# Kernel optimization log

Hardware: AMD Instinct MI355X
Metric: run time of the kernel (lower is better)

The kernel has to match this reference:

```python
import jax, jax.numpy as jnp
import numpy as np

N_NODES = 50000
N_EDGES = 600000
D = 128


def setup_inputs() -> dict:
    key = jax.random.key(0)
    k = jax.random.split(key, 6)
    x = jax.random.normal(k[0], (N_NODES, D), dtype=jnp.float32)
    edge_src = jax.random.randint(k[1], (N_EDGES,), 0, N_NODES, dtype=jnp.int64 if jax.config.jax_enable_x64 else jnp.int32)
    edge_dst = jax.random.randint(k[2], (N_EDGES,), 0, N_NODES, dtype=jnp.int64 if jax.config.jax_enable_x64 else jnp.int32)
    # message MLP: [h_src ; h_dst] (2D) -> D, update MLP: [h ; agg] (2D) -> D
    scale = 1.0 / np.sqrt(2 * D)
    W1 = jax.random.normal(k[3], (2 * D, D), dtype=jnp.float32) * scale
    b1 = jnp.zeros((D,), dtype=jnp.float32)
    W2 = jax.random.normal(k[4], (2 * D, D), dtype=jnp.float32) * scale
    b2 = jnp.zeros((D,), dtype=jnp.float32)
    return {"x": x, "edge_src": edge_src, "edge_dst": edge_dst,
            "W1": W1, "b1": b1, "W2": W2, "b2": b2}


def reference(x, edge_src, edge_dst, W1, b1, W2, b2):
    # gather endpoint features per edge: [E, 2D]
    pair = jnp.concatenate([x[edge_src], x[edge_dst]], axis=-1)
    # per-edge message MLP: [E, D]
    msg = jax.nn.relu(pair @ W1 + b1)
    # scatter-aggregate (sum) messages into destination nodes: [N, D]
    agg = jax.ops.segment_sum(msg, edge_dst, num_segments=N_NODES)
    # node update MLP with residual: [N, D]
    upd = jax.nn.relu(jnp.concatenate([x, agg], axis=-1) @ W2 + b2)
    return x + upd
```

## Files before the change

### kernel.cpp

```cpp
#include <hip/hip_runtime.h>
#include <stdint.h>


typedef __attribute__((ext_vector_type(8))) short short8;
typedef __attribute__((ext_vector_type(4))) float floatx4;

#define D 128

static __device__ __forceinline__ unsigned short f2bf(float f) {
    union { float f; unsigned int u; } v; v.f = f;
    unsigned int r = (v.u + 0x7fffu + ((v.u >> 16) & 1u)) >> 16;
    return (unsigned short)r;
}
static __device__ __forceinline__ float bflo(unsigned int u) {
    union { unsigned int u; float f; } v; v.u = u << 16; return v.f;
}
static __device__ __forceinline__ float bfhi(unsigned int u) {
    union { unsigned int u; float f; } v; v.u = u & 0xffff0000u; return v.f;
}

__global__ void k_convert_w(const float* __restrict__ W1, const float* __restrict__ W2,
                            unsigned short* __restrict__ w1f, unsigned short* __restrict__ w2f,
                            int* __restrict__ cursor, int N) {
    int gid = blockIdx.x * blockDim.x + threadIdx.x;
    if (gid < N) cursor[gid] = 0;
    if (gid < 32768) {
        int tid = gid;
        int j = tid & 7, lane = (tid >> 3) & 63, ct = (tid >> 9) & 15, kk = tid >> 13;
        int k = kk * 32 + (lane >> 4) * 8 + j;
        int c = ((ct >> 2) << 6) + ((lane & 15) << 2) + (ct & 3);
        float v = (c < 128) ? W1[k * 128 + c] : W1[(128 + k) * 128 + (c - 128)];
        w1f[tid] = f2bf(v);
    } else {
        int tid = gid - 32768;
        int j = tid & 7, lane = (tid >> 3) & 63, ct = (tid >> 9) & 7, kk = tid >> 12;
        int k = kk * 32 + (lane >> 4) * 8 + j;
        int c = ((ct >> 1) << 5) + ((lane & 15) << 1) + (ct & 1);
        w2f[tid] = f2bf(W2[k * 128 + c]);
    }
}

__global__ __launch_bounds__(256) void k_gemm1(
    const float* __restrict__ x,
    const unsigned short* __restrict__ w1f,
    const float* __restrict__ b1,
    unsigned short* __restrict__ xb,
    unsigned short* __restrict__ Ys,
    unsigned short* __restrict__ Yd,
    int N, int nTiles)
{
    const int tid = threadIdx.x, w = tid >> 6, lane = tid & 63;
    const int quad = lane >> 4, col = lane & 15;

    short8 wf[4][4];
#pragma unroll
    for (int kk = 0; kk < 4; kk++)
#pragma unroll
        for (int j = 0; j < 4; j++)
            wf[kk][j] = ((const short8*)w1f)[(kk * 16 + w * 4 + j) * 64 + lane];
    float4 bias = make_float4(0.f, 0.f, 0.f, 0.f);
    if (w >= 2) bias = *(const float4*)(b1 + (w - 2) * 64 + col * 4);
    unsigned short* Yhalf = (w < 2) ? Ys : Yd;
    const int cb = (w & 1) * 64;

    for (int t = blockIdx.x; t < nTiles; t += gridDim.x) {
        const int n0 = t * 16;
        const int nr = n0 + col;
        const float* xrow = x + (long)nr * D;
        floatx4 acc[4];
#pragma unroll
        for (int j = 0; j < 4; j++)
#pragma unroll
            for (int q = 0; q < 4; q++) acc[j][q] = 0.f;
#pragma unroll
        for (int kk = 0; kk < 4; kk++) {
            float4 f0 = *(const float4*)(xrow + kk * 32 + quad * 8);
            float4 f1 = *(const float4*)(xrow + kk * 32 + quad * 8 + 4);
            union { short8 s; unsigned int u[4]; } au;
            asm("v_cvt_pk_bf16_f32 %0, %1, %2" : "=v"(au.u[0]) : "v"(f0.x), "v"(f0.y));
            asm("v_cvt_pk_bf16_f32 %0, %1, %2" : "=v"(au.u[1]) : "v"(f0.z), "v"(f0.w));
            asm("v_cvt_pk_bf16_f32 %0, %1, %2" : "=v"(au.u[2]) : "v"(f1.x), "v"(f1.y));
            asm("v_cvt_pk_bf16_f32 %0, %1, %2" : "=v"(au.u[3]) : "v"(f1.z), "v"(f1.w));
            if (w == 0)
                *(short8*)(xb + (long)nr * D + kk * 32 + quad * 8) = au.s;
#pragma unroll
            for (int j = 0; j < 4; j++)
                acc[j] = __builtin_amdgcn_mfma_f32_16x16x32_bf16(au.s, wf[kk][j], acc[j], 0, 0, 0);
        }
#pragma unroll
        for (int r = 0; r < 4; r++) {
            int n = n0 + quad * 4 + r;
            ushort4 o;
            o.x = f2bf(acc[0][r] + bias.x);
            o.y = f2bf(acc[1][r] + bias.y);
            o.z = f2bf(acc[2][r] + bias.z);
            o.w = f2bf(acc[3][r] + bias.w);
            *(ushort4*)(Yhalf + (long)n * D + cb + col * 4) = o;
        }
    }
}

__global__ void k_hist(const int* __restrict__ dst, int* __restrict__ cnt, int E) {
    int i = blockIdx.x * blockDim.x + threadIdx.x;
    if (i < E) atomicAdd(&cnt[dst[i]], 1);
}

__global__ void k_scanA(const int* __restrict__ cnt, int* __restrict__ rowptr,
                        int* __restrict__ bsum, int N) {
    __shared__ int ws[16];
    int tid = threadIdx.x, i = blockIdx.x * 1024 + tid;
    int lane = tid & 63, wv = tid >> 6;
    int c = (i < N) ? cnt[i] : 0;
    int incl = c;
#pragma unroll
    for (int off = 1; off < 64; off <<= 1) {
        int t = __shfl_up(incl, off, 64);
        if (lane >= off) incl += t;
    }
    if (lane == 63) ws[wv] = incl;
    __syncthreads();
    if (wv == 0) {
        int v = (lane < 16) ? ws[lane] : 0;
        int s = v;
#pragma unroll
        for (int off = 1; off < 16; off <<= 1) {
            int t = __shfl_up(s, off, 64);
            if (lane >= off) s += t;
        }
        if (lane < 16) ws[lane] = s - v;
    }
    __syncthreads();
    if (i < N) rowptr[i] = incl - c + ws[wv];
    if (tid == 1023) bsum[blockIdx.x] = ws[15] + incl;
}

__global__ void k_scanC(int* __restrict__ rowptr, int* __restrict__ cursor,
                        const int* __restrict__ bsum, int N, int E, int nb) {
    __shared__ int off_s;
    int tid = threadIdx.x;
    int chunk = blockIdx.x >> 2;
    if (tid < 64) {
        int v = (tid < chunk && tid < nb) ? bsum[tid] : 0;
#pragma unroll
        for (int off = 32; off; off >>= 1) v += __shfl_down(v, off, 64);
        if (tid == 0) off_s = v;
    }
    __syncthreads();
    int i = blockIdx.x * 256 + tid;
    if (i < N) {
        int r = rowptr[i] + off_s;
        rowptr[i] = r;
        cursor[i] = r;
    }
    if (i == 0) rowptr[N] = E;
}

__global__ void k_scatter(const int* __restrict__ src, const int* __restrict__ dst,
                          int* __restrict__ cursor, int* __restrict__ ssrc, int E) {
    int i = blockIdx.x * blockDim.x + threadIdx.x;
    if (i < E) {
        int p = atomicAdd(&cursor[dst[i]], 1);
        ssrc[p] = src[i];
    }
}

__global__ __launch_bounds__(256) void k_agg(
    const unsigned short* __restrict__ Ys,
    const unsigned short* __restrict__ Yd,
    const int* __restrict__ rowptr,
    const int* __restrict__ ssrc,
    unsigned short* __restrict__ aggb, int N)
{
    int wv = blockIdx.x * 4 + (threadIdx.x >> 6);
    if (wv >= N) return;
    int lane = threadIdx.x & 63;
    int rp0 = rowptr[wv], rp1 = rowptr[wv + 1];
    unsigned int ydu = *(const unsigned int*)(Yd + (long)wv * D + lane * 2);
    float yd0 = bflo(ydu), yd1 = bfhi(ydu);
    float a0 = 0.f, a1 = 0.f;
    const unsigned short* ysl = Ys + lane * 2;
    int e = rp0;
    for (; e + 8 <= rp1; e += 8) {
        int s[8]; unsigned int u[8];
#pragma unroll
        for (int q = 0; q < 8; q++) s[q] = ssrc[e + q];
#pragma unroll
        for (int q = 0; q < 8; q++) u[q] = *(const unsigned int*)(ysl + (long)s[q] * D);
#pragma unroll
        for (int q = 0; q < 8; q++) {
            a0 += fmaxf(bflo(u[q]) + yd0, 0.f);
            a1 += fmaxf(bfhi(u[q]) + yd1, 0.f);
        }
    }
    for (; e + 4 <= rp1; e += 4) {
        int s[4]; unsigned int u[4];
#pragma unroll
        for (int q = 0; q < 4; q++) s[q] = ssrc[e + q];
#pragma unroll
        for (int q = 0; q < 4; q++) u[q] = *(const unsigned int*)(ysl + (long)s[q] * D);
#pragma unroll
        for (int q = 0; q < 4; q++) {
            a0 += fmaxf(bflo(u[q]) + yd0, 0.f);
            a1 += fmaxf(bfhi(u[q]) + yd1, 0.f);
        }
    }
    for (; e < rp1; e++) {
        unsigned int u0 = *(const unsigned int*)(ysl + (long)ssrc[e] * D);
        a0 += fmaxf(bflo(u0) + yd0, 0.f);
        a1 += fmaxf(bfhi(u0) + yd1, 0.f);
    }
    unsigned int o = (unsigned int)f2bf(a0) | ((unsigned int)f2bf(a1) << 16);
    *(unsigned int*)(aggb + (long)wv * D + lane * 2) = o;
}

__global__ __launch_bounds__(256) void k_gemm2(
    const unsigned short* __restrict__ xb,
    const unsigned short* __restrict__ aggb,
    const unsigned short* __restrict__ w2f,
    const float* __restrict__ b2,
    const float* __restrict__ x,
    float* __restrict__ out,
    int N, int nTiles)
{
    const int tid = threadIdx.x, w = tid >> 6, lane = tid & 63;
    const int quad = lane >> 4, col = lane & 15;

    short8 wf[8][2];
#pragma unroll
    for (int kk = 0; kk < 8; kk++)
#pragma unroll
        for (int c = 0; c < 2; c++)
            wf[kk][c] = ((const short8*)w2f)[(kk * 8 + w * 2 + c) * 64 + lane];
    float2 bias = *(const float2*)(b2 + w * 32 + col * 2);

    for (int t = blockIdx.x; t < nTiles; t += gridDim.x) {
        const int n0 = t * 16;
        const int nr = n0 + col;
        floatx4 acc[2];
#pragma unroll
        for (int c = 0; c < 2; c++)
#pragma unroll
            for (int q = 0; q < 4; q++) acc[c][q] = 0.f;
#pragma unroll
        for (int kk = 0; kk < 8; kk++) {
            const unsigned short* base = (kk < 4) ? xb : aggb;
            short8 a = *(const short8*)(base + (long)nr * D + (kk & 3) * 32 + quad * 8);
            acc[0] = __builtin_amdgcn_mfma_f32_16x16x32_bf16(a, wf[kk][0], acc[0], 0, 0, 0);
            acc[1] = __builtin_amdgcn_mfma_f32_16x16x32_bf16(a, wf[kk][1], acc[1], 0, 0, 0);
        }
#pragma unroll
        for (int r = 0; r < 4; r++) {
            int n = n0 + quad * 4 + r;
            long off = (long)n * D + w * 32 + col * 2;
            float2 xr = *(const float2*)(x + off);
            float v0 = fmaxf(acc[0][r] + bias.x, 0.f);
            float v1 = fmaxf(acc[1][r] + bias.y, 0.f);
            *(float2*)(out + off) = make_float2(xr.x + v0, xr.y + v1);
        }
    }
}

extern "C" void kernel_launch(void* const* d_in, const int* in_sizes, int n_in,
                              void* d_out, int out_size, void* d_ws, size_t ws_size,
                              hipStream_t stream)
{
    const float* x   = (const float*)d_in[0];
    const int* esrc  = (const int*)d_in[1];
    const int* edst  = (const int*)d_in[2];
    const float* W1  = (const float*)d_in[3];
    const float* b1  = (const float*)d_in[4];
    const float* W2  = (const float*)d_in[5];
    const float* b2  = (const float*)d_in[6];
    float* out = (float*)d_out;

    const int ND = in_sizes[0];
    const int N  = ND / D;
    const int E  = in_sizes[1];

    char* p = (char*)d_ws;
    auto alloc = [&](size_t bytes) { char* r = p; p += (bytes + 255) & ~(size_t)255; return r; };
    unsigned short* Ys   = (unsigned short*)alloc((size_t)ND * 2);
    unsigned short* Yd   = (unsigned short*)alloc((size_t)ND * 2);
    unsigned short* xb   = (unsigned short*)alloc((size_t)ND * 2);
    unsigned short* aggb = (unsigned short*)alloc((size_t)ND * 2);
    unsigned short* w1f  = (unsigned short*)alloc(32768 * 2);
    unsigned short* w2f  = (unsigned short*)alloc(32768 * 2);
    int* rowptr = (int*)alloc((size_t)(N + 1) * 4);
    int* cursor = (int*)alloc((size_t)N * 4);
    int* bsum   = (int*)alloc(64 * 4);
    int* ssrc   = (int*)alloc((size_t)E * 4);

    const int nTiles = N / 16;
    const int nb = (N + 1023) / 1024;

    k_convert_w<<<256, 256, 0, stream>>>(W1, W2, w1f, w2f, cursor, N);
    k_gemm1<<<1024, 256, 0, stream>>>(x, w1f, b1, xb, Ys, Yd, N, nTiles);
    k_hist<<<(E + 255) / 256, 256, 0, stream>>>(edst, cursor, E);
    k_scanA<<<nb, 1024, 0, stream>>>(cursor, rowptr, bsum, N);
    k_scanC<<<(N + 255) / 256, 256, 0, stream>>>(rowptr, cursor, bsum, N, E, nb);
    k_scatter<<<(E + 255) / 256, 256, 0, stream>>>(esrc, edst, cursor, ssrc, E);
    k_agg<<<(N + 3) / 4, 256, 0, stream>>>(Ys, Yd, rowptr, ssrc, aggb, N);
    k_gemm2<<<1024, 256, 0, stream>>>(xb, aggb, w2f, b2, x, out, N, nTiles);
}
```

Measured before the change: 211.9 us.

## Fuse histogram into GEMM1 grid, single-block scan, vectorized scatter, drop xb buffer

Runs the in-degree histogram on extra blocks of the first GEMM kernel so both proceed concurrently. The two-kernel scan becomes a single 1024-thread block that handles 52 entries per thread. The scatter and histogram now read edges as int4. The bf16 copy of x is no longer stored; GEMM2 reconverts x from fp32 itself. Grid sizes change to about a third of the tiles. Together this cuts launch count and intermediate traffic, at the cost of a serial single-block scan and extra fp32 reads in GEMM2.

```diff
diff --git a/kernel.cpp b/kernel.cpp
--- a/kernel.cpp
+++ b/kernel.cpp
@@ -19,11 +19,11 @@
     union { unsigned int u; float f; } v; v.u = u & 0xffff0000u; return v.f;
 }
 
-__global__ void k_convert_w(const float* __restrict__ W1, const float* __restrict__ W2,
-                            unsigned short* __restrict__ w1f, unsigned short* __restrict__ w2f,
-                            int* __restrict__ cursor, int N) {
+__global__ void k_pre(const float* __restrict__ W1, const float* __restrict__ W2,
+                      unsigned short* __restrict__ w1f, unsigned short* __restrict__ w2f,
+                      int* __restrict__ cnt, int N) {
     int gid = blockIdx.x * blockDim.x + threadIdx.x;
-    if (gid < N) cursor[gid] = 0;
+    if (gid < N) cnt[gid] = 0;
     if (gid < 32768) {
         int tid = gid;
         int j = tid & 7, lane = (tid >> 3) & 63, ct = (tid >> 9) & 15, kk = tid >> 13;
@@ -40,16 +40,33 @@
     }
 }
 
-__global__ __launch_bounds__(256) void k_gemm1(
+__global__ __launch_bounds__(256) void k_fat1(
     const float* __restrict__ x,
     const unsigned short* __restrict__ w1f,
     const float* __restrict__ b1,
-    unsigned short* __restrict__ xb,
     unsigned short* __restrict__ Ys,
     unsigned short* __restrict__ Yd,
-    int N, int nTiles)
+    const int* __restrict__ edst,
+    int* __restrict__ cnt,
+    int N, int nTiles, int nb1, int E)
 {
-    const int tid = threadIdx.x, w = tid >> 6, lane = tid & 63;
+    const int tid = threadIdx.x;
+    if ((int)blockIdx.x >= nb1) {
+        const int hthreads = (gridDim.x - nb1) * 256;
+        const int hid = (blockIdx.x - nb1) * 256 + tid;
+        const int E4 = E >> 2;
+        for (int i = hid; i < E4; i += hthreads) {
+            int4 d = ((const int4*)edst)[i];
+            atomicAdd(&cnt[d.x], 1);
+            atomicAdd(&cnt[d.y], 1);
+            atomicAdd(&cnt[d.z], 1);
+            atomicAdd(&cnt[d.w], 1);
+        }
+        for (int i = (E4 << 2) + hid; i < E; i += hthreads)
+            atomicAdd(&cnt[edst[i]], 1);
+        return;
+    }
+    const int w = tid >> 6, lane = tid & 63;
     const int quad = lane >> 4, col = lane & 15;
 
     short8 wf[4][4];
@@ -63,7 +80,7 @@
     unsigned short* Yhalf = (w < 2) ? Ys : Yd;
     const int cb = (w & 1) * 64;
 
-    for (int t = blockIdx.x; t < nTiles; t += gridDim.x) {
+    for (int t = blockIdx.x; t < nTiles; t += nb1) {
         const int n0 = t * 16;
         const int nr = n0 + col;
         const float* xrow = x + (long)nr * D;
@@ -81,8 +98,6 @@
             asm("v_cvt_pk_bf16_f32 %0, %1, %2" : "=v"(au.u[1]) : "v"(f0.z), "v"(f0.w));
             asm("v_cvt_pk_bf16_f32 %0, %1, %2" : "=v"(au.u[2]) : "v"(f1.x), "v"(f1.y));
             asm("v_cvt_pk_bf16_f32 %0, %1, %2" : "=v"(au.u[3]) : "v"(f1.z), "v"(f1.w));
-            if (w == 0)
-                *(short8*)(xb + (long)nr * D + kk * 32 + quad * 8) = au.s;
 #pragma unroll
             for (int j = 0; j < 4; j++)
                 acc[j] = __builtin_amdgcn_mfma_f32_16x16x32_bf16(au.s, wf[kk][j], acc[j], 0, 0, 0);
@@ -100,18 +115,25 @@
     }
 }
 
-__global__ void k_hist(const int* __restrict__ dst, int* __restrict__ cnt, int E) {
-    int i = blockIdx.x * blockDim.x + threadIdx.x;
-    if (i < E) atomicAdd(&cnt[dst[i]], 1);
-}
-
-__global__ void k_scanA(const int* __restrict__ cnt, int* __restrict__ rowptr,
-                        int* __restrict__ bsum, int N) {
+__global__ __launch_bounds__(1024) void k_scan(const int* __restrict__ cnt,
+                                               int* __restrict__ rowptr,
+                                               int* __restrict__ cursor, int N, int E) {
     __shared__ int ws[16];
-    int tid = threadIdx.x, i = blockIdx.x * 1024 + tid;
-    int lane = tid & 63, wv = tid >> 6;
-    int c = (i < N) ? cnt[i] : 0;
-    int incl = c;
+    const int tid = threadIdx.x, lane = tid & 63, wv = tid >> 6;
+    const int base = tid * 52;
+    int sum = 0;
+#pragma unroll
+    for (int q = 0; q < 13; q++) {
+        int i = base + q * 4;
+        if (i + 3 < N) {
+            int4 c = *(const int4*)(cnt + i);
+            sum += c.x + c.y + c.z + c.w;
+        } else {
+#pragma unroll
+            for (int r = 0; r < 4; r++) if (i + r < N) sum += cnt[i + r];
+        }
+    }
+    int incl = sum;
 #pragma unroll
     for (int off = 1; off < 64; off <<= 1) {
         int t = __shfl_up(incl, off, 64);
@@ -130,37 +152,41 @@
         if (lane < 16) ws[lane] = s - v;
     }
     __syncthreads();
-    if (i < N) rowptr[i] = incl - c + ws[wv];
-    if (tid == 1023) bsum[blockIdx.x] = ws[15] + incl;
-}
-
-__global__ void k_scanC(int* __restrict__ rowptr, int* __restrict__ cursor,
-                        const int* __restrict__ bsum, int N, int E, int nb) {
-    __shared__ int off_s;
-    int tid = threadIdx.x;
-    int chunk = blockIdx.x >> 2;
-    if (tid < 64) {
-        int v = (tid < chunk && tid < nb) ? bsum[tid] : 0;
-#pragma unroll
-        for (int off = 32; off; off >>= 1) v += __shfl_down(v, off, 64);
-        if (tid == 0) off_s = v;
-    }
-    __syncthreads();
-    int i = blockIdx.x * 256 + tid;
-    if (i < N) {
-        int r = rowptr[i] + off_s;
-        rowptr[i] = r;
-        cursor[i] = r;
-    }
-    if (i == 0) rowptr[N] = E;
+    int run = incl - sum + ws[wv];
+#pragma unroll
+    for (int q = 0; q < 13; q++) {
+        int i = base + q * 4;
+        if (i + 3 < N) {
+            int4 c = *(const int4*)(cnt + i);
+            int4 o = make_int4(run, run + c.x, run + c.x + c.y, run + c.x + c.y + c.z);
+            *(int4*)(rowptr + i) = o;
+            *(int4*)(cursor + i) = o;
+            run += c.x + c.y + c.z + c.w;
+        } else {
+#pragma unroll
+            for (int r = 0; r < 4; r++)
+                if (i + r < N) { rowptr[i + r] = run; cursor[i + r] = run; run += cnt[i + r]; }
+        }
+    }
+    if (tid == 0) rowptr[N] = E;
 }
 
 __global__ void k_scatter(const int* __restrict__ src, const int* __restrict__ dst,
                           int* __restrict__ cursor, int* __restrict__ ssrc, int E) {
     int i = blockIdx.x * blockDim.x + threadIdx.x;
-    if (i < E) {
-        int p = atomicAdd(&cursor[dst[i]], 1);
-        ssrc[p] = src[i];
+    const int E4 = E >> 2;
+    if (i < E4) {
+        int4 s = ((const int4*)src)[i];
+        int4 d = ((const int4*)dst)[i];
+        int p0 = atomicAdd(&cursor[d.x], 1); ssrc[p0] = s.x;
+        int p1 = atomicAdd(&cursor[d.y], 1); ssrc[p1] = s.y;
+        int p2 = atomicAdd(&cursor[d.z], 1); ssrc[p2] = s.z;
+        int p3 = atomicAdd(&cursor[d.w], 1); ssrc[p3] = s.w;
+    }
+    if (i < (E & 3)) {
+        int e = (E4 << 2) + i;
+        int p = atomicAdd(&cursor[dst[e]], 1);
+        ssrc[p] = src[e];
     }
 }
 
@@ -214,13 +240,12 @@
 }
 
 __global__ __launch_bounds__(256) void k_gemm2(
-    const unsigned short* __restrict__ xb,
+    const float* __restrict__ x,
     const unsigned short* __restrict__ aggb,
     const unsigned short* __restrict__ w2f,
     const float* __restrict__ b2,
-    const float* __restrict__ x,
     float* __restrict__ out,
-    int N, int nTiles)
+    int N, int nTiles, int nb2)
 {
     const int tid = threadIdx.x, w = tid >> 6, lane = tid & 63;
     const int quad = lane >> 4, col = lane & 15;
@@ -233,18 +258,30 @@
             wf[kk][c] = ((const short8*)w2f)[(kk * 8 + w * 2 + c) * 64 + lane];
     float2 bias = *(const float2*)(b2 + w * 32 + col * 2);
 
-    for (int t = blockIdx.x; t < nTiles; t += gridDim.x) {
+    for (int t = blockIdx.x; t < nTiles; t += nb2) {
         const int n0 = t * 16;
         const int nr = n0 + col;
+        const float* xrow = x + (long)nr * D;
         floatx4 acc[2];
 #pragma unroll
         for (int c = 0; c < 2; c++)
 #pragma unroll
             for (int q = 0; q < 4; q++) acc[c][q] = 0.f;
 #pragma unroll
-        for (int kk = 0; kk < 8; kk++) {
-            const unsigned short* base = (kk < 4) ? xb : aggb;
-            short8 a = *(const short8*)(base + (long)nr * D + (kk & 3) * 32 + quad * 8);
+        for (int kk = 0; kk < 4; kk++) {
+            float4 f0 = *(const float4*)(xrow + kk * 32 + quad * 8);
+            float4 f1 = *(const float4*)(xrow + kk * 32 + quad * 8 + 4);
+            union { short8 s; unsigned int u[4]; } au;
+            asm("v_cvt_pk_bf16_f32 %0, %1, %2" : "=v"(au.u[0]) : "v"(f0.x), "v"(f0.y));
+            asm("v_cvt_pk_bf16_f32 %0, %1, %2" : "=v"(au.u[1]) : "v"(f0.z), "v"(f0.w));
+            asm("v_cvt_pk_bf16_f32 %0, %1, %2" : "=v"(au.u[2]) : "v"(f1.x), "v"(f1.y));
+            asm("v_cvt_pk_bf16_f32 %0, %1, %2" : "=v"(au.u[3]) : "v"(f1.z), "v"(f1.w));
+            acc[0] = __builtin_amdgcn_mfma_f32_16x16x32_bf16(au.s, wf[kk][0], acc[0], 0, 0, 0);
+            acc[1] = __builtin_amdgcn_mfma_f32_16x16x32_bf16(au.s, wf[kk][1], acc[1], 0, 0, 0);
+        }
+#pragma unroll
+        for (int kk = 4; kk < 8; kk++) {
+            short8 a = *(const short8*)(aggb + (long)nr * D + (kk - 4) * 32 + quad * 8);
             acc[0] = __builtin_amdgcn_mfma_f32_16x16x32_bf16(a, wf[kk][0], acc[0], 0, 0, 0);
             acc[1] = __builtin_amdgcn_mfma_f32_16x16x32_bf16(a, wf[kk][1], acc[1], 0, 0, 0);
         }
@@ -281,24 +318,23 @@
     auto alloc = [&](size_t bytes) { char* r = p; p += (bytes + 255) & ~(size_t)255; return r; };
     unsigned short* Ys   = (unsigned short*)alloc((size_t)ND * 2);
     unsigned short* Yd   = (unsigned short*)alloc((size_t)ND * 2);
-    unsigned short* xb   = (unsigned short*)alloc((size_t)ND * 2);
     unsigned short* aggb = (unsigned short*)alloc((size_t)ND * 2);
     unsigned short* w1f  = (unsigned short*)alloc(32768 * 2);
     unsigned short* w2f  = (unsigned short*)alloc(32768 * 2);
     int* rowptr = (int*)alloc((size_t)(N + 1) * 4);
     int* cursor = (int*)alloc((size_t)N * 4);
-    int* bsum   = (int*)alloc(64 * 4);
+    int* cnt    = (int*)alloc((size_t)N * 4);
     int* ssrc   = (int*)alloc((size_t)E * 4);
 
     const int nTiles = N / 16;
-    const int nb = (N + 1023) / 1024;
-
-    k_convert_w<<<256, 256, 0, stream>>>(W1, W2, w1f, w2f, cursor, N);
-    k_gemm1<<<1024, 256, 0, stream>>>(x, w1f, b1, xb, Ys, Yd, N, nTiles);
-    k_hist<<<(E + 255) / 256, 256, 0, stream>>>(edst, cursor, E);
-    k_scanA<<<nb, 1024, 0, stream>>>(cursor, rowptr, bsum, N);
-    k_scanC<<<(N + 255) / 256, 256, 0, stream>>>(rowptr, cursor, bsum, N, E, nb);
-    k_scatter<<<(E + 255) / 256, 256, 0, stream>>>(esrc, edst, cursor, ssrc, E);
+    const int nb1 = (nTiles + 2) / 3;
+    const int nbh = 256;
+    const int nb2 = nb1;
+
+    k_pre<<<256, 256, 0, stream>>>(W1, W2, w1f, w2f, cnt, N);
+    k_fat1<<<nb1 + nbh, 256, 0, stream>>>(x, w1f, b1, Ys, Yd, edst, cnt, N, nTiles, nb1, E);
+    k_scan<<<1, 1024, 0, stream>>>(cnt, rowptr, cursor, N, E);
+    k_scatter<<<((E >> 2) + 255) / 256, 256, 0, stream>>>(esrc, edst, cursor, ssrc, E);
     k_agg<<<(N + 3) / 4, 256, 0, stream>>>(Ys, Yd, rowptr, ssrc, aggb, N);
-    k_gemm2<<<1024, 256, 0, stream>>>(xb, aggb, w2f, b2, x, out, N, nTiles);
-}
+    k_gemm2<<<nb2, 256, 0, stream>>>(x, aggb, w2f, b2, out, N, nTiles, nb2);
+}
```

After: 245.9 us. 1.16x slower.
